# Performance work log

Hardware: AMD Instinct MI355X
Metric: run time of the kernel (lower is better)

Reference implementation:

```python
import jax, jax.numpy as jnp
import numpy as np
import math

DIM = 2048
N_HEADS = 16
HEAD_DIM = DIM // N_HEADS  # 128
SEQ = 2048
EPS = 1e-5
NEG = -1e9


def get_slopes(n):
    # n is a power of 2 here (16)
    start = 2.0 ** (-2.0 ** (-(math.log2(n) - 3)))
    return [start * start ** i for i in range(n)]


def setup_inputs() -> dict:
    key = jax.random.key(0)
    ks = jax.random.split(key, 6)
    x = jax.random.normal(ks[0], (1, SEQ, DIM), dtype=jnp.float32)
    # causal additive mask (large negative above diagonal)
    causal = jnp.tril(jnp.ones((SEQ, SEQ), dtype=bool))
    mask = jnp.where(causal, 0.0, NEG).astype(jnp.float32)[None, None]
    scale_w = 0.02
    wq = jax.random.normal(ks[1], (DIM, DIM), dtype=jnp.float32) * scale_w  # [in, out]
    wk = jax.random.normal(ks[2], (DIM, DIM), dtype=jnp.float32) * scale_w
    wv = jax.random.normal(ks[3], (DIM, DIM), dtype=jnp.float32) * scale_w
    wo = jax.random.normal(ks[4], (DIM, DIM), dtype=jnp.float32) * scale_w
    # AttentionPrior params: shape_init=1, scale_init='slope' (stored as log), loc_init=0
    shape = jnp.ones((1, N_HEADS, 1, 1), dtype=jnp.float32)
    scale = jnp.log(jnp.asarray(get_slopes(N_HEADS), dtype=jnp.float32)).reshape(1, N_HEADS, 1, 1)
    loc = jnp.zeros((1, N_HEADS, 1, 1), dtype=jnp.float32)
    return {"x": x, "mask": mask, "wq": wq, "wk": wk, "wv": wv, "wo": wo,
            "shape": shape, "scale": scale, "loc": loc, "start_pos": 0}


def _prior_bias(shape, scale, loc, seqlen, start_pos):
    q_pos = jnp.arange(seqlen, dtype=jnp.float32) + start_pos
    k_pos = jnp.arange(seqlen + start_pos, dtype=jnp.float32)
    dist = (k_pos[None, :] - q_pos[:, None])[None, None]  # [1,1,S,K]
    loc_t = jnp.exp(loc) - jnp.exp(-loc)
    z = (dist - loc_t) * jnp.exp(scale)  # [1,H,S,K]
    return -(jnp.abs(z) + EPS) ** shape


def reference(x, mask, wq, wk, wv, wo, shape, scale, loc, start_pos):
    bsz, seqlen, _ = x.shape
    q = (x @ wq).reshape(bsz, seqlen, N_HEADS, HEAD_DIM)
    k = (x @ wk).reshape(bsz, seqlen, N_HEADS, HEAD_DIM)
    v = (x @ wv).reshape(bsz, seqlen, N_HEADS, HEAD_DIM)
    # start_pos=0 prefill: cache slice == current keys/values
    scores = jnp.einsum('bqhd,bkhd->bhqk', q, k) / math.sqrt(HEAD_DIM)
    scores = scores + _prior_bias(shape, scale, loc, seqlen, start_pos)
    scores = scores + mask
    probs = jax.nn.softmax(scores.astype(jnp.float32), axis=-1).astype(q.dtype)
    out = jnp.einsum('bhqk,bkhd->bqhd', probs, v).reshape(bsz, seqlen, DIM)
    return out @ wo
```

## Files before the change

### kernel.cpp

```cpp
#include <hip/hip_runtime.h>
#include <hip/hip_bf16.h>
#include <stdint.h>


typedef unsigned short u16;
typedef unsigned int u32;

using bf16x8 = __attribute__((ext_vector_type(8))) __bf16;
using f32x4  = __attribute__((ext_vector_type(4))) float;

__device__ __forceinline__ u16 f2bf(float f) {
  union { float f; u32 u; } v; v.f = f;
  u32 r = (v.u + 0x7FFFu + ((v.u >> 16) & 1u)) >> 16;
  return (u16)r;
}

__device__ __forceinline__ float bf2f(u16 h) {
  union { u32 u; float f; } v; v.u = ((u32)h) << 16; return v.f;
}

__device__ __forceinline__ void gload16(const void* g, void* l) {
  __builtin_amdgcn_global_load_lds((const __attribute__((address_space(1))) void*)g,
                                   (__attribute__((address_space(3))) void*)l, 16, 0, 0);
}

__device__ __forceinline__ int cumchunks(int qt) {
  if (qt < 8)  return qt;
  if (qt < 16) return 8 + 2 * (qt - 8);
  if (qt < 24) return 24 + 3 * (qt - 16);
  return 48 + 4 * (qt - 24);
}

__global__ __launch_bounds__(256) void convx(const float* __restrict__ x, u16* __restrict__ xb) {
  int i = blockIdx.x * 256 + threadIdx.x;
  float4 v = ((const float4*)x)[i];
  ushort4 o;
  o.x = f2bf(v.x); o.y = f2bf(v.y); o.z = f2bf(v.z); o.w = f2bf(v.w);
  ((ushort4*)xb)[i] = o;
}

__global__ __launch_bounds__(256) void transw(const float* __restrict__ wq, const float* __restrict__ wk,
                                              const float* __restrict__ wv, const float* __restrict__ wo,
                                              u16* __restrict__ wqkt, u16* __restrict__ wvt,
                                              u16* __restrict__ wot) {
  __shared__ float tile[32][33];
  const int z = blockIdx.z;
  const float* src = (z == 0) ? wq : (z == 1) ? wk : (z == 2) ? wv : wo;
  u16* dst = (z == 0) ? wqkt : (z == 1) ? (wqkt + 2048 * 2048) : (z == 2) ? wvt : wot;
  const int c0 = blockIdx.x * 32, r0 = blockIdx.y * 32;
  const int t = threadIdx.x;
  const int ci = t & 31, rj = t >> 5;
#pragma unroll
  for (int j = 0; j < 4; ++j)
    tile[rj + j * 8][ci] = src[(size_t)(r0 + rj + j * 8) * 2048 + c0 + ci];
  __syncthreads();
#pragma unroll
  for (int j = 0; j < 4; ++j) {
    int rr = rj + j * 8;
    dst[(size_t)(c0 + rr) * 2048 + r0 + ci] = f2bf(tile[ci][rr]);
  }
}

__global__ __launch_bounds__(256) void gemm_qkv(const u16* __restrict__ xb, const u16* __restrict__ wqkt,
                                                const u16* __restrict__ wvt,
                                                u16* __restrict__ qkc, u16* __restrict__ vtc) {
  __shared__ u16 lds[16384];
  const int raw = blockIdx.x;
  int bid = (raw & 7) * 96 + (raw >> 3);
  const u16 *A, *Bt;
  u16* C;
  int N, bn, bm, scl_cols;
  if (bid < 512) { A = xb;  Bt = wqkt; C = qkc; N = 4096; bn = bid & 31; bm = bid >> 5; scl_cols = 2048; }
  else { bid -= 512; A = wvt; Bt = xb; C = vtc; N = 2048; bn = bid & 15; bm = bid >> 4; scl_cols = 0; }
  const int K = 2048;

  const int t = threadIdx.x;
  const int w = t >> 6, l = t & 63;
  const int wm = w >> 1, wn = w & 1;
  const int lrow = l & 15, lgrp = l >> 4;

  f32x4 acc[4][4] = {};

  for (int k0 = 0; k0 < K; k0 += 64) {
    if (k0) __syncthreads();
#pragma unroll
    for (int p = 0; p < 4; ++p) {
      int i = (p * 4 + w) * 64 + l;
      int r = i >> 3, u = i & 7;
      const u16* src = A + (size_t)(bm * 128 + r) * K + k0 + ((u ^ (r & 7)) << 3);
      gload16(src, (char*)lds + (p * 4 + w) * 1024);
    }
#pragma unroll
    for (int p = 0; p < 4; ++p) {
      int i = (p * 4 + w) * 64 + l;
      int r = i >> 3, u = i & 7;
      const u16* src = Bt + (size_t)(bn * 128 + r) * K + k0 + ((u ^ (r & 7)) << 3);
      gload16(src, (char*)lds + 16384 + (p * 4 + w) * 1024);
    }
    __syncthreads();

#pragma unroll
    for (int kc = 0; kc < 2; ++kc) {
      bf16x8 af[4], bfr[4];
#pragma unroll
      for (int mt = 0; mt < 4; ++mt) {
        int rho = wm * 64 + mt * 16 + lrow;
        int un = (kc * 4 + lgrp) ^ (rho & 7);
        af[mt] = *(const bf16x8*)((const char*)lds + rho * 128 + un * 16);
      }
#pragma unroll
      for (int nt = 0; nt < 4; ++nt) {
        int rho = wn * 64 + nt * 16 + lrow;
        int un = (kc * 4 + lgrp) ^ (rho & 7);
        bfr[nt] = *(const bf16x8*)((const char*)lds + 16384 + rho * 128 + un * 16);
      }
#pragma unroll
      for (int mt = 0; mt < 4; ++mt)
#pragma unroll
        for (int nt = 0; nt < 4; ++nt)
          acc[mt][nt] = __builtin_amdgcn_mfma_f32_16x16x32_bf16(af[mt], bfr[nt], acc[mt][nt], 0, 0, 0);
    }
  }

  const int row0 = bm * 128 + wm * 64;
  const int col0 = bn * 128 + wn * 64;
#pragma unroll
  for (int mt = 0; mt < 4; ++mt)
#pragma unroll
    for (int nt = 0; nt < 4; ++nt) {
      int col = col0 + nt * 16 + lrow;
      float s = (col < scl_cols) ? 0.08838834764831843f : 1.0f;
#pragma unroll
      for (int r = 0; r < 4; ++r) {
        int row = row0 + mt * 16 + lgrp * 4 + r;
        C[(size_t)row * N + col] = f2bf(acc[mt][nt][r] * s);
      }
    }
}

__global__ __launch_bounds__(256) void gemm_outk(const u16* __restrict__ A, const u16* __restrict__ Bt,
                                                 u16* __restrict__ P0, u16* __restrict__ P1) {
  __shared__ u16 lds[16384];
  const int raw = blockIdx.x;
  const int b = (raw & 7) * 64 + (raw >> 3);
  const int z = b >> 8;
  const int bn = b & 15, bm = (b >> 4) & 15;
  u16* C = z ? P1 : P0;
  const int K = 2048;
  const int kbeg = z * 1024, kend = kbeg + 1024;

  const int t = threadIdx.x;
  const int w = t >> 6, l = t & 63;
  const int wm = w >> 1, wn = w & 1;
  const int lrow = l & 15, lgrp = l >> 4;

  f32x4 acc[4][4] = {};

  for (int k0 = kbeg; k0 < kend; k0 += 64) {
    if (k0 != kbeg) __syncthreads();
#pragma unroll
    for (int p = 0; p < 4; ++p) {
      int i = (p * 4 + w) * 64 + l;
      int r = i >> 3, u = i & 7;
      const u16* src = A + (size_t)(bm * 128 + r) * K + k0 + ((u ^ (r & 7)) << 3);
      gload16(src, (char*)lds + (p * 4 + w) * 1024);
    }
#pragma unroll
    for (int p = 0; p < 4; ++p) {
      int i = (p * 4 + w) * 64 + l;
      int r = i >> 3, u = i & 7;
      const u16* src = Bt + (size_t)(bn * 128 + r) * K + k0 + ((u ^ (r & 7)) << 3);
      gload16(src, (char*)lds + 16384 + (p * 4 + w) * 1024);
    }
    __syncthreads();

#pragma unroll
    for (int kc = 0; kc < 2; ++kc) {
      bf16x8 af[4], bfr[4];
#pragma unroll
      for (int mt = 0; mt < 4; ++mt) {
        int rho = wm * 64 + mt * 16 + lrow;
        int un = (kc * 4 + lgrp) ^ (rho & 7);
        af[mt] = *(const bf16x8*)((const char*)lds + rho * 128 + un * 16);
      }
#pragma unroll
      for (int nt = 0; nt < 4; ++nt) {
        int rho = wn * 64 + nt * 16 + lrow;
        int un = (kc * 4 + lgrp) ^ (rho & 7);
        bfr[nt] = *(const bf16x8*)((const char*)lds + 16384 + rho * 128 + un * 16);
      }
#pragma unroll
      for (int mt = 0; mt < 4; ++mt)
#pragma unroll
        for (int nt = 0; nt < 4; ++nt)
          acc[mt][nt] = __builtin_amdgcn_mfma_f32_16x16x32_bf16(af[mt], bfr[nt], acc[mt][nt], 0, 0, 0);
    }
  }

  const int row0 = bm * 128 + wm * 64;
  const int col0 = bn * 128 + wn * 64;
#pragma unroll
  for (int mt = 0; mt < 4; ++mt)
#pragma unroll
    for (int nt = 0; nt < 4; ++nt) {
      int col = col0 + nt * 16 + lrow;
#pragma unroll
      for (int r = 0; r < 4; ++r) {
        int row = row0 + mt * 16 + lgrp * 4 + r;
        C[(size_t)row * 2048 + col] = f2bf(acc[mt][nt][r]);
      }
    }
}

__global__ __launch_bounds__(256) void combine_out(const u16* __restrict__ P0, const u16* __restrict__ P1,
                                                   float* __restrict__ out) {
  const int i = blockIdx.x * 256 + threadIdx.x;
  uint4 a = ((const uint4*)P0)[i];
  uint4 b = ((const uint4*)P1)[i];
  float4 o0, o1;
  o0.x = bf2f(a.x & 0xFFFF) + bf2f(b.x & 0xFFFF); o0.y = bf2f(a.x >> 16) + bf2f(b.x >> 16);
  o0.z = bf2f(a.y & 0xFFFF) + bf2f(b.y & 0xFFFF); o0.w = bf2f(a.y >> 16) + bf2f(b.y >> 16);
  o1.x = bf2f(a.z & 0xFFFF) + bf2f(b.z & 0xFFFF); o1.y = bf2f(a.z >> 16) + bf2f(b.z >> 16);
  o1.z = bf2f(a.w & 0xFFFF) + bf2f(b.w & 0xFFFF); o1.w = bf2f(a.w >> 16) + bf2f(b.w >> 16);
  ((float4*)out)[i * 2]     = o0;
  ((float4*)out)[i * 2 + 1] = o1;
}

__global__ __launch_bounds__(256) void attn_part(const u16* __restrict__ QK, const u16* __restrict__ Vt,
                                                 u16* __restrict__ Opart, float* __restrict__ Lpart,
                                                 const float* __restrict__ g_shape,
                                                 const float* __restrict__ g_scale,
                                                 const float* __restrict__ g_loc,
                                                 const int* __restrict__ g_sp) {
  __shared__ u16 k_lds[2][8192];
  __shared__ u16 v_lds[2][8192];
  __shared__ u16 p_lds[4][1152];

  const int raw = blockIdx.x;
  const int bid = (raw & 7) * 160 + (raw >> 3);
  const int h = bid / 80;
  const int rem = bid - h * 80;
  int qt, ch;
  if (rem < 8)       { qt = rem;                 ch = 0; }
  else if (rem < 24) { int r2 = rem - 8;  qt = 8  + (r2 >> 1); ch = r2 & 1; }
  else if (rem < 48) { int r3 = rem - 24; qt = 16 + r3 / 3;    ch = r3 - 3 * (r3 / 3); }
  else               { int r4 = rem - 48; qt = 24 + (r4 >> 2); ch = r4 & 3; }
  const int pid = bid;

  const int t = threadIdx.x, w = t >> 6, l = t & 63;
  const int lrow = l & 15, lgrp = l >> 4;

  const float sh = g_shape[h];
  const float es = __expf(g_scale[h]);
  const float lcv = g_loc[h];
  const float loc_t = __expf(lcv) - __expf(-lcv);
  const int sp = g_sp[0];
  const bool shape1 = (sh == 1.0f);

  const int qbase = qt * 64 + w * 16;

  bf16x8 qf[4];
  {
    const u16* qp = QK + (size_t)(qbase + lrow) * 4096 + h * 128 + lgrp * 8;
#pragma unroll
    for (int kc = 0; kc < 4; ++kc) qf[kc] = *(const bf16x8*)(qp + kc * 32);
  }

  f32x4 o[8] = {};
  float lr[4] = {0.0f, 0.0f, 0.0f, 0.0f};

  const int kstart = ch * 8;
  const int kend = min(kstart + 8, qt + 1);

#define STAGE_TILE(buf, kt_) do {                                                        \
    const int kv0s = (kt_) * 64;                                                         \
    _Pragma("unroll")                                                                    \
    for (int p = 0; p < 4; ++p) {                                                        \
      int i = (p * 4 + w) * 64 + l;                                                      \
      int r = i >> 4, u = i & 15;                                                        \
      const u16* src = QK + (size_t)(kv0s + r) * 4096 + 2048 + h * 128 + ((u ^ (r & 7)) << 3); \
      gload16(src, (char*)k_lds[buf] + (p * 4 + w) * 1024);                              \
    }                                                                                    \
    _Pragma("unroll")                                                                    \
    for (int p = 0; p < 4; ++p) {                                                        \
      int i = (p * 4 + w) * 64 + l;                                                      \
      int r = i >> 3, u = i & 7;                                                         \
      const u16* src = Vt + (size_t)(h * 128 + r) * 2048 + kv0s + ((u ^ (r & 7)) << 3);  \
      gload16(src, (char*)v_lds[buf] + (p * 4 + w) * 1024);                              \
    }                                                                                    \
  } while (0)

  STAGE_TILE(0, kstart);
  __syncthreads();

  for (int kt = kstart; kt < kend; ++kt) {
    const int cur = (kt - kstart) & 1;
    if (kt + 1 < kend) STAGE_TILE(cur ^ 1, kt + 1);
    const int kv0 = kt * 64;

    f32x4 s4[4];
#pragma unroll
    for (int nc = 0; nc < 4; ++nc) s4[nc] = f32x4{-11.0f, -11.0f, -11.0f, -11.0f};
#pragma unroll
    for (int kc = 0; kc < 4; ++kc) {
#pragma unroll
      for (int nc = 0; nc < 4; ++nc) {
        int rho = nc * 16 + lrow;
        int un = (kc * 4 + lgrp) ^ (rho & 7);
        bf16x8 bk = *(const bf16x8*)((const char*)k_lds[cur] + rho * 256 + un * 16);
        s4[nc] = __builtin_amdgcn_mfma_f32_16x16x32_bf16(qf[kc], bk, s4[nc], 0, 0, 0);
      }
    }

    f32x4 p4[4];
    const bool need_mask = (kv0 + 63 > qbase + sp);
    if (shape1 && !need_mask) {
#pragma unroll
      for (int r = 0; r < 4; ++r) {
        const float fb = (float)(kv0 + lrow - (qbase + lgrp * 4 + r) - sp) - loc_t;
#pragma unroll
        for (int nc = 0; nc < 4; ++nc) {
          float u = fb + (float)(nc * 16);
          float p = __expf(fmaf(-es, fabsf(u), s4[nc][r]));
          p4[nc][r] = p;
          lr[r] += p;
        }
      }
    } else if (shape1) {
#pragma unroll
      for (int r = 0; r < 4; ++r) {
        const float fb = (float)(kv0 + lrow - (qbase + lgrp * 4 + r) - sp) - loc_t;
#pragma unroll
        for (int nc = 0; nc < 4; ++nc) {
          float u = fb + (float)(nc * 16);
          float p = __expf(fmaf(-es, fabsf(u), s4[nc][r]));
          p = (u + loc_t > 0.0f) ? 0.0f : p;
          p4[nc][r] = p;
          lr[r] += p;
        }
      }
    } else {
#pragma unroll
      for (int r = 0; r < 4; ++r) {
        const float fb = (float)(kv0 + lrow - (qbase + lgrp * 4 + r) - sp) - loc_t;
#pragma unroll
        for (int nc = 0; nc < 4; ++nc) {
          float u = fb + (float)(nc * 16);
          float az = fmaf(es, fabsf(u), 1e-5f);
          float p = __expf(s4[nc][r] - __powf(az, sh));
          p = (u + loc_t > 0.0f) ? 0.0f : p;
          p4[nc][r] = p;
          lr[r] += p;
        }
      }
    }

#pragma unroll
    for (int r = 0; r < 4; ++r)
#pragma unroll
      for (int nc = 0; nc < 4; ++nc)
        p_lds[w][(lgrp * 4 + r) * 72 + nc * 16 + lrow] = f2bf(p4[nc][r]);

#pragma unroll
    for (int ks = 0; ks < 2; ++ks) {
      bf16x8 pa = *(const bf16x8*)((const char*)p_lds[w] + lrow * 144 + ks * 64 + lgrp * 16);
#pragma unroll
      for (int dc = 0; dc < 8; ++dc) {
        int rho = dc * 16 + lrow;
        int un = (ks * 4 + lgrp) ^ (rho & 7);
        bf16x8 bv = *(const bf16x8*)((const char*)v_lds[cur] + rho * 128 + un * 16);
        o[dc] = __builtin_amdgcn_mfma_f32_16x16x32_bf16(pa, bv, o[dc], 0, 0, 0);
      }
    }

    __syncthreads();
  }
#undef STAGE_TILE

#pragma unroll
  for (int r = 0; r < 4; ++r)
#pragma unroll
    for (int msk = 1; msk <= 8; msk <<= 1) lr[r] += __shfl_xor(lr[r], msk);

  u16* ob = Opart + (size_t)pid * 8192;
#pragma unroll
  for (int dc = 0; dc < 8; ++dc) {
#pragma unroll
    for (int r = 0; r < 4; ++r) {
      int row = w * 16 + lgrp * 4 + r;
      ob[(size_t)row * 128 + dc * 16 + lrow] = f2bf(o[dc][r]);
    }
  }
  if (lrow == 0) {
#pragma unroll
    for (int r = 0; r < 4; ++r) {
      int row = w * 16 + lgrp * 4 + r;
      Lpart[(size_t)pid * 64 + row] = lr[r];
    }
  }
}

__global__ __launch_bounds__(256) void attn_merge(const u16* __restrict__ Opart,
                                                  const float* __restrict__ Lpart,
                                                  u16* __restrict__ AO) {
  const int bid = blockIdx.x;
  const int qt = bid & 31, h = bid >> 5;
  const int nch = (qt >> 3) + 1;
  const int base = h * 80 + cumchunks(qt);
  const int t = threadIdx.x;
  const int row = t >> 2;
  const int dseg = (t & 3) << 5;

  float acc[32] = {};
  float lstar = 0.0f;
#pragma unroll
  for (int i = 0; i < 4; ++i) {
    if (i < nch) {
      lstar += Lpart[(size_t)(base + i) * 64 + row];
      const ushort4* op = (const ushort4*)(Opart + (size_t)(base + i) * 8192 + row * 128 + dseg);
#pragma unroll
      for (int j = 0; j < 8; ++j) {
        ushort4 v = op[j];
        acc[j * 4 + 0] += bf2f(v.x); acc[j * 4 + 1] += bf2f(v.y);
        acc[j * 4 + 2] += bf2f(v.z); acc[j * 4 + 3] += bf2f(v.w);
      }
    }
  }
  const float inv = 1.0f / lstar;
  const int q_abs = qt * 64 + row;
  u16* dst = AO + (size_t)q_abs * 2048 + h * 128 + dseg;
#pragma unroll
  for (int j = 0; j < 8; ++j) {
    ushort4 ov;
    ov.x = f2bf(acc[j * 4 + 0] * inv); ov.y = f2bf(acc[j * 4 + 1] * inv);
    ov.z = f2bf(acc[j * 4 + 2] * inv); ov.w = f2bf(acc[j * 4 + 3] * inv);
    *(ushort4*)(dst + j * 4) = ov;
  }
}

extern "C" void kernel_launch(void* const* d_in, const int* in_sizes, int n_in,
                              void* d_out, int out_size, void* d_ws, size_t ws_size,
                              hipStream_t stream) {
  const float* x   = (const float*)d_in[0];
  const float* wq  = (const float*)d_in[2];
  const float* wk  = (const float*)d_in[3];
  const float* wv  = (const float*)d_in[4];
  const float* wo  = (const float*)d_in[5];
  const float* shp = (const float*)d_in[6];
  const float* scl = (const float*)d_in[7];
  const float* loc = (const float*)d_in[8];
  const int*   sp  = (const int*)d_in[9];

  char* ws = (char*)d_ws;
  u16*   xb    = (u16*)(ws);
  u16*   wqkt  = (u16*)(ws + (size_t)( 8u << 20));
  u16*   wvt   = (u16*)(ws + (size_t)(24u << 20));
  u16*   opart = (u16*)(ws);
  u16*   wot   = (u16*)(ws + (size_t)(40u << 20));
  u16*   qk    = (u16*)(ws + (size_t)(48u << 20));
  u16*   pc0   = (u16*)(ws + (size_t)(48u << 20));
  u16*   pc1   = (u16*)(ws + (size_t)(56u << 20));
  u16*   vt    = (u16*)(ws + (size_t)(64u << 20));
  u16*   ao    = (u16*)(ws + (size_t)(72u << 20));
  float* lpart = (float*)(ws + (size_t)(80u << 20));

  hipLaunchKernelGGL(convx, dim3(4096), dim3(256), 0, stream, x, xb);
  hipLaunchKernelGGL(transw, dim3(64, 64, 4), dim3(256), 0, stream, wq, wk, wv, wo, wqkt, wvt, wot);
  hipLaunchKernelGGL(gemm_qkv, dim3(768), dim3(256), 0, stream, xb, wqkt, wvt, qk, vt);
  hipLaunchKernelGGL(attn_part, dim3(1280), dim3(256), 0, stream,
                     qk, vt, opart, lpart, shp, scl, loc, sp);
  hipLaunchKernelGGL(attn_merge, dim3(512), dim3(256), 0, stream, opart, lpart, ao);
  hipLaunchKernelGGL(gemm_outk, dim3(512), dim3(256), 0, stream, ao, wot, pc0, pc1);
  hipLaunchKernelGGL(combine_out, dim3(2048), dim3(256), 0, stream, pc0, pc1, (float*)d_out);
}
```

Baseline: 172.8 us.

## Load K/V fragments directly from global memory in attention, drop LDS staging

The attention kernel stops staging K and V tiles into double-buffered LDS and instead has each wave read its MFMA operands straight from global memory. This removes the LDS traffic and the per-tile block barrier. In exchange, each of the four waves fetches the same K/V data separately, which relies on L2/L1 caching and adds uncoalesced 16-byte loads with no prefetch overlap. The GEMM kernels also drop their XCD-aware block-index remapping and use blockIdx directly.

```diff
diff --git a/kernel.cpp b/kernel.cpp
--- a/kernel.cpp
+++ b/kernel.cpp
@@ -65,8 +65,7 @@
                                                 const u16* __restrict__ wvt,
                                                 u16* __restrict__ qkc, u16* __restrict__ vtc) {
   __shared__ u16 lds[16384];
-  const int raw = blockIdx.x;
-  int bid = (raw & 7) * 96 + (raw >> 3);
+  int bid = blockIdx.x;
   const u16 *A, *Bt;
   u16* C;
   int N, bn, bm, scl_cols;
@@ -141,8 +140,7 @@
 __global__ __launch_bounds__(256) void gemm_outk(const u16* __restrict__ A, const u16* __restrict__ Bt,
                                                  u16* __restrict__ P0, u16* __restrict__ P1) {
   __shared__ u16 lds[16384];
-  const int raw = blockIdx.x;
-  const int b = (raw & 7) * 64 + (raw >> 3);
+  const int b = blockIdx.x;
   const int z = b >> 8;
   const int bn = b & 15, bm = (b >> 4) & 15;
   u16* C = z ? P1 : P0;
@@ -232,8 +230,6 @@
                                                  const float* __restrict__ g_scale,
                                                  const float* __restrict__ g_loc,
                                                  const int* __restrict__ g_sp) {
-  __shared__ u16 k_lds[2][8192];
-  __shared__ u16 v_lds[2][8192];
   __shared__ u16 p_lds[4][1152];
 
   const int raw = blockIdx.x;
@@ -272,44 +268,26 @@
   const int kstart = ch * 8;
   const int kend = min(kstart + 8, qt + 1);
 
-#define STAGE_TILE(buf, kt_) do {                                                        \
-    const int kv0s = (kt_) * 64;                                                         \
-    _Pragma("unroll")                                                                    \
-    for (int p = 0; p < 4; ++p) {                                                        \
-      int i = (p * 4 + w) * 64 + l;                                                      \
-      int r = i >> 4, u = i & 15;                                                        \
-      const u16* src = QK + (size_t)(kv0s + r) * 4096 + 2048 + h * 128 + ((u ^ (r & 7)) << 3); \
-      gload16(src, (char*)k_lds[buf] + (p * 4 + w) * 1024);                              \
-    }                                                                                    \
-    _Pragma("unroll")                                                                    \
-    for (int p = 0; p < 4; ++p) {                                                        \
-      int i = (p * 4 + w) * 64 + l;                                                      \
-      int r = i >> 3, u = i & 7;                                                         \
-      const u16* src = Vt + (size_t)(h * 128 + r) * 2048 + kv0s + ((u ^ (r & 7)) << 3);  \
-      gload16(src, (char*)v_lds[buf] + (p * 4 + w) * 1024);                              \
-    }                                                                                    \
-  } while (0)
-
-  STAGE_TILE(0, kstart);
-  __syncthreads();
+  const u16* kb = QK + 2048 + h * 128 + lgrp * 8 + (size_t)(lrow)*4096;
+  const u16* vb = Vt + (size_t)h * 128 * 2048 + lgrp * 8;
 
   for (int kt = kstart; kt < kend; ++kt) {
-    const int cur = (kt - kstart) & 1;
-    if (kt + 1 < kend) STAGE_TILE(cur ^ 1, kt + 1);
     const int kv0 = kt * 64;
 
     f32x4 s4[4];
 #pragma unroll
     for (int nc = 0; nc < 4; ++nc) s4[nc] = f32x4{-11.0f, -11.0f, -11.0f, -11.0f};
 #pragma unroll
-    for (int kc = 0; kc < 4; ++kc) {
-#pragma unroll
-      for (int nc = 0; nc < 4; ++nc) {
-        int rho = nc * 16 + lrow;
-        int un = (kc * 4 + lgrp) ^ (rho & 7);
-        bf16x8 bk = *(const bf16x8*)((const char*)k_lds[cur] + rho * 256 + un * 16);
-        s4[nc] = __builtin_amdgcn_mfma_f32_16x16x32_bf16(qf[kc], bk, s4[nc], 0, 0, 0);
-      }
+    for (int nc = 0; nc < 4; ++nc) {
+      const u16* kr = kb + (size_t)(kv0 + nc * 16) * 4096;
+      bf16x8 bk0 = *(const bf16x8*)(kr);
+      bf16x8 bk1 = *(const bf16x8*)(kr + 32);
+      bf16x8 bk2 = *(const bf16x8*)(kr + 64);
+      bf16x8 bk3 = *(const bf16x8*)(kr + 96);
+      s4[nc] = __builtin_amdgcn_mfma_f32_16x16x32_bf16(qf[0], bk0, s4[nc], 0, 0, 0);
+      s4[nc] = __builtin_amdgcn_mfma_f32_16x16x32_bf16(qf[1], bk1, s4[nc], 0, 0, 0);
+      s4[nc] = __builtin_amdgcn_mfma_f32_16x16x32_bf16(qf[2], bk2, s4[nc], 0, 0, 0);
+      s4[nc] = __builtin_amdgcn_mfma_f32_16x16x32_bf16(qf[3], bk3, s4[nc], 0, 0, 0);
     }
 
     f32x4 p4[4];
@@ -366,16 +344,12 @@
       bf16x8 pa = *(const bf16x8*)((const char*)p_lds[w] + lrow * 144 + ks * 64 + lgrp * 16);
 #pragma unroll
       for (int dc = 0; dc < 8; ++dc) {
-        int rho = dc * 16 + lrow;
-        int un = (ks * 4 + lgrp) ^ (rho & 7);
-        bf16x8 bv = *(const bf16x8*)((const char*)v_lds[cur] + rho * 128 + un * 16);
+        const u16* vr = vb + (size_t)(dc * 16 + lrow) * 2048 + kv0 + ks * 32;
+        bf16x8 bv = *(const bf16x8*)vr;
         o[dc] = __builtin_amdgcn_mfma_f32_16x16x32_bf16(pa, bv, o[dc], 0, 0, 0);
       }
     }
-
-    __syncthreads();
-  }
-#undef STAGE_TILE
+  }
 
 #pragma unroll
   for (int r = 0; r < 4; ++r)
```

Measured after the change: 293.7 us. 70.0% more time.
